# Kernel tuning notes

Hardware: AMD Instinct MI355X
Metric: run time of the kernel (lower is better)

Reference implementation:

```python
import jax, jax.numpy as jnp
import numpy as np

N_AST, M, C, D, H, OUT = 200000, 400000, 25000, 256, 4, 256


def setup_inputs() -> dict:
    key = jax.random.key(0)
    ks = jax.random.split(key, 12)
    s = 0.02
    return {
        "ast_nodes_encodings": jax.random.normal(ks[0], (N_AST, D), jnp.float32),
        "ast_node_idx_to_pdg_node_idx_mapping_key": jax.random.randint(ks[1], (M,), 0, N_AST),
        "ast_node_idx_to_pdg_node_idx_mapping_value": jax.random.randint(ks[2], (M,), 0, C),
        "pdg_node_idx_to_sub_ast_root_idx_mapping_key": jax.random.randint(ks[3], (C,), 0, C),
        "pdg_node_idx_to_sub_ast_root_idx_mapping_value": jax.random.randint(ks[4], (C,), 0, N_AST),
        "nr_cfg_nodes": C,
        "Wq": jax.random.normal(ks[5], (D, D), jnp.float32) * s,
        "bq": jnp.zeros((D,), jnp.float32),
        "Wk": jax.random.normal(ks[6], (D, D), jnp.float32) * s,
        "bk": jnp.zeros((D,), jnp.float32),
        "Wv": jax.random.normal(ks[7], (D, D), jnp.float32) * s,
        "bv": jnp.zeros((D,), jnp.float32),
        "Wo": jax.random.normal(ks[8], (D, OUT), jnp.float32) * s,
        "bo": jnp.zeros((OUT,), jnp.float32),
    }


def _scatter_attn(x, attn_keys, seg, num_segments, Wq, bq, Wk, bk, Wv, bv, Wo, bo):
    # x: [M, D] scattered inputs; attn_keys: [C, D] per-segment queries; seg: [M] segment ids.
    d_h = D // H
    q = (attn_keys @ Wq + bq).reshape(num_segments, H, d_h)  # [C,H,dh]
    k = (x @ Wk + bk).reshape(-1, H, d_h)                    # [M,H,dh]
    v = (x @ Wv + bv).reshape(-1, H, d_h)                    # [M,H,dh]
    scale = 1.0 / jnp.sqrt(jnp.asarray(d_h, x.dtype))
    scores = jnp.einsum('mhd,mhd->mh', k, q[seg]) * scale    # [M,H]
    m = jax.ops.segment_max(scores, seg, num_segments=num_segments)  # [C,H]
    e = jnp.exp(scores - m[seg])                             # [M,H]
    denom = jax.ops.segment_sum(e, seg, num_segments=num_segments)  # [C,H]
    num = jax.ops.segment_sum((e[..., None] * v).reshape(-1, H * d_h),
                              seg, num_segments=num_segments)        # [C,D]
    pooled = (num.reshape(num_segments, H, d_h) / (denom[..., None] + 1e-9)).reshape(num_segments, D)
    return pooled @ Wo + bo                                  # [C,OUT]


def reference(ast_nodes_encodings,
              ast_node_idx_to_pdg_node_idx_mapping_key,
              ast_node_idx_to_pdg_node_idx_mapping_value,
              pdg_node_idx_to_sub_ast_root_idx_mapping_key,
              pdg_node_idx_to_sub_ast_root_idx_mapping_value,
              nr_cfg_nodes, Wq, bq, Wk, bk, Wv, bv, Wo, bo):
    # Build per-CFG-node attention keys: gather sub-AST-root encodings, scatter by PDG node idx.
    root_enc = ast_nodes_encodings[pdg_node_idx_to_sub_ast_root_idx_mapping_value]  # [C,D]
    attn_keys = jnp.zeros((nr_cfg_nodes, D), ast_nodes_encodings.dtype)
    attn_keys = attn_keys.at[pdg_node_idx_to_sub_ast_root_idx_mapping_key].set(root_enc)
    # Gather AST node encodings per mapping entry and attention-pool per CFG node.
    scattered = ast_nodes_encodings[ast_node_idx_to_pdg_node_idx_mapping_key]       # [M,D]
    return _scatter_attn(scattered, attn_keys, ast_node_idx_to_pdg_node_idx_mapping_value,
                         nr_cfg_nodes, Wq, bq, Wk, bk, Wv, bv, Wo, bo)
```

## Files before the change

### kernel.cpp

```cpp
#include <hip/hip_runtime.h>
#include <hip/hip_bf16.h>
#include <math.h>

#define D 256
#define H 4
#define DH 64
#define NOUT 256

typedef short bf16x8 __attribute__((ext_vector_type(8)));
typedef float f32x4 __attribute__((ext_vector_type(4)));

__device__ __forceinline__ ushort f2bf(float f){
  uint b = __float_as_uint(f);
  b += 0x7FFF + ((b >> 16) & 1);
  return (ushort)(b >> 16);
}
__device__ __forceinline__ float bf2f(ushort u){
  return __uint_as_float(((uint)u) << 16);
}

__device__ __forceinline__ float redux32(float v){
  int t;
  t = __builtin_amdgcn_update_dpp(0, __float_as_int(v), 0x121, 0xF, 0xF, true); v += __int_as_float(t);
  t = __builtin_amdgcn_update_dpp(0, __float_as_int(v), 0x122, 0xF, 0xF, true); v += __int_as_float(t);
  t = __builtin_amdgcn_update_dpp(0, __float_as_int(v), 0x124, 0xF, 0xF, true); v += __int_as_float(t);
  t = __builtin_amdgcn_update_dpp(0, __float_as_int(v), 0x128, 0xF, 0xF, true); v += __int_as_float(t);
  v += __shfl_xor(v, 16, 64);
  return v;
}

__global__ void count_winner_kernel(const int* __restrict__ seg, int* __restrict__ counts,
                                    const int* __restrict__ pdgkey, int* __restrict__ winner,
                                    int M, int C){
  int i = blockIdx.x*256 + threadIdx.x;
  if (i < M){ int s = seg[i]; if (s >= 0 && s < C) atomicAdd(&counts[s], 1); }
  if (i < C){ int t = pdgkey[i]; if (t >= 0 && t < C) atomicMax(&winner[t], i); }
}

__global__ __launch_bounds__(1024) void scan1_kernel(const int* __restrict__ counts,
    int* __restrict__ loc, int* __restrict__ btot, int C){
  __shared__ int wtot[16];
  __shared__ int wexcl[16];
  int tid = threadIdx.x, lane = tid & 63, wv = tid >> 6;
  int i = blockIdx.x*1024 + tid;
  int v = (i < C) ? counts[i] : 0;
  int x = v;
  #pragma unroll
  for (int d2 = 1; d2 < 64; d2 <<= 1){
    int t = __shfl_up(x, d2, 64);
    if (lane >= d2) x += t;
  }
  if (lane == 63) wtot[wv] = x;
  __syncthreads();
  if (wv == 0 && lane < 16){
    int t = wtot[lane]; int y = t;
    #pragma unroll
    for (int d2 = 1; d2 < 16; d2 <<= 1){
      int u = __shfl_up(y, d2, 64);
      if (lane >= d2) y += u;
    }
    wexcl[lane] = y - t;
    if (lane == 15) btot[blockIdx.x] = y;
  }
  __syncthreads();
  if (i < C) loc[i] = wexcl[wv] + x - v;
}

__global__ void scan2_kernel(const int* __restrict__ btot, int* __restrict__ bexcl,
                             int nb, int* __restrict__ offsets, int C){
  int lane = threadIdx.x;
  int v = (lane < nb) ? btot[lane] : 0;
  int x = v;
  #pragma unroll
  for (int d2 = 1; d2 < 64; d2 <<= 1){
    int t = __shfl_up(x, d2, 64);
    if (lane >= d2) x += t;
  }
  if (lane < nb) bexcl[lane] = x - v;
  if (lane == 63) offsets[C] = x;
}

__global__ void scan3_kernel(const int* __restrict__ loc, const int* __restrict__ bexcl,
                             int* __restrict__ offsets, int* __restrict__ pos, int C){
  int i = blockIdx.x*256 + threadIdx.x;
  if (i < C){ int o = loc[i] + bexcl[i >> 10]; offsets[i] = o; pos[i] = o; }
}

__global__ void fill_kernel(const int* __restrict__ seg, const int* __restrict__ astkey,
                            int* __restrict__ pos, int* __restrict__ rows, int M, int C){
  int i = blockIdx.x*256 + threadIdx.x;
  if (i < M){
    int s = seg[i];
    if (s >= 0 && s < C){ int p = atomicAdd(&pos[s], 1); rows[p] = astkey[i]; }
  }
}

__global__ __launch_bounds__(256) void prep_weights(
    const float* __restrict__ Wq, const float* __restrict__ Wk,
    const float* __restrict__ Wv, const float* __restrict__ Wo,
    const float* __restrict__ bq, const float* __restrict__ bk,
    const float* __restrict__ bv,
    ushort* __restrict__ Wq16, ushort* __restrict__ Wk16, ushort* __restrict__ Wv16,
    ushort* __restrict__ WoT16,
    float* __restrict__ wqbk, float* __restrict__ bvo,
    float* __restrict__ bqk, float* __restrict__ cbh){
  __shared__ float t[64][65];
  int bid = blockIdx.x, tid = threadIdx.x;
  if (bid < 256){
    int id = bid*256 + tid;
    Wq16[id] = f2bf(Wq[id]);
    Wk16[id] = f2bf(Wk[id]);
    Wv16[id] = f2bf(Wv[id]);
  } else if (bid < 269){
    int id = (bid - 256)*256 + tid;
    if (id < 1024){
      int h = id >> 8, k = id & 255;
      float s = 0.f;
      for (int d = 0; d < DH; d++) s += Wq[(size_t)k*256 + h*64 + d] * bk[h*64 + d];
      wqbk[id] = s;
    } else if (id < 2048){
      int tt = id - 1024; int h = tt >> 8, o = tt & 255;
      float s = 0.f;
      for (int d = 0; d < DH; d++) s += bv[h*64 + d] * Wo[(size_t)(h*64 + d)*256 + o];
      bvo[tt] = s;
    } else if (id < 3072){
      int tt = id - 2048; int h = tt >> 8, e = tt & 255;
      float s = 0.f;
      for (int d = 0; d < DH; d++) s += bq[h*64 + d] * Wk[(size_t)e*256 + h*64 + d];
      bqk[tt] = s;
    } else if (id < 3076){
      int h = id - 3072;
      float s = 0.f;
      for (int d = 0; d < DH; d++) s += bq[h*64 + d] * bk[h*64 + d];
      cbh[h] = s;
    }
  } else {
    int b2 = bid - 269;
    int bx = b2 & 3, by = b2 >> 2;
    int r = tid >> 6, cc = tid & 63;
    #pragma unroll
    for (int rr = 0; rr < 64; rr += 4)
      t[rr + r][cc] = Wo[(size_t)(by*64 + rr + r)*256 + bx*64 + cc];
    __syncthreads();
    #pragma unroll
    for (int rr = 0; rr < 64; rr += 4)
      WoT16[(size_t)(bx*64 + rr + r)*256 + by*64 + cc] = f2bf(t[cc][rr + r]);
  }
}

__global__ void gather_ag(const float* __restrict__ enc, const int* __restrict__ rootval,
                          const int* __restrict__ winner,
                          const float* __restrict__ wqbk, const float* __restrict__ cbh,
                          ushort* __restrict__ Ag, float* __restrict__ qb, int C){
  int id = blockIdx.x*256 + threadIdx.x;
  int c = id >> 6, g = id & 63;
  if (c >= C) return;
  int w = winner[c];
  float4 v = make_float4(0.f, 0.f, 0.f, 0.f);
  if (w >= 0) v = *(const float4*)(enc + (size_t)rootval[w]*D + g*4);
  ushort4 u; u.x = f2bf(v.x); u.y = f2bf(v.y); u.z = f2bf(v.z); u.w = f2bf(v.w);
  *(ushort4*)(Ag + (size_t)c*D + g*4) = u;
  float b0 = bf2f(u.x), b1 = bf2f(u.y), b2 = bf2f(u.z), b3 = bf2f(u.w);
  float pv[4];
  #pragma unroll
  for (int h = 0; h < 4; h++){
    float4 wv = *(const float4*)(wqbk + h*256 + g*4);
    float p = b0*wv.x + b1*wv.y + b2*wv.z + b3*wv.w;
    p = redux32(p);
    p += __shfl_xor(p, 32, 64);
    pv[h] = p;
  }
  if (g < 4) qb[c*4 + g] = pv[g] + cbh[g];
}

template<bool OUT_BF16>
__global__ __launch_bounds__(256) void mfma_gemm(
    const ushort* __restrict__ A, int sA, int acol_h,
    const ushort* __restrict__ Bt, int sBt, int btrow_h, int btcol_h,
    void* __restrict__ Out, int sOut, int outrow_h, int outcol_h,
    int M, int K,
    const float* __restrict__ bias, const float* __restrict__ beta4,
    const float* __restrict__ bvo4){
  __shared__ __align__(16) ushort As[64][72];
  __shared__ __align__(16) ushort Bs[64][72];
  int tid = threadIdx.x;
  int hz = blockIdx.z;
  int m0 = blockIdx.x*64;
  int acol0  = acol_h*hz;
  int btrow0 = blockIdx.y*64 + btrow_h*hz;
  int btcol0 = btcol_h*hz;
  int outrow0 = outrow_h*hz;
  int outcol0 = blockIdx.y*64 + outcol_h*hz;
  int w = tid >> 6, lane = tid & 63, quad = lane >> 4, l16 = lane & 15;
  int r1 = tid >> 3, c8 = (tid & 7)*8;
  f32x4 acc[4] = {};
  for (int k0 = 0; k0 < K; k0 += 64){
    const ushort* ga = A + (size_t)(m0 + r1)*sA + acol0 + k0 + c8;
    uint4 v1 = make_uint4(0,0,0,0), v2 = make_uint4(0,0,0,0);
    if (m0 + r1 < M)      v1 = *(const uint4*)ga;
    if (m0 + r1 + 32 < M) v2 = *(const uint4*)(ga + (size_t)32*sA);
    *(uint4*)&As[r1][c8]      = v1;
    *(uint4*)&As[r1+32][c8]   = v2;
    const ushort* gb = Bt + (size_t)(btrow0 + r1)*sBt + btcol0 + k0 + c8;
    *(uint4*)&Bs[r1][c8]      = *(const uint4*)gb;
    *(uint4*)&Bs[r1+32][c8]   = *(const uint4*)(gb + (size_t)32*sBt);
    __syncthreads();
    #pragma unroll
    for (int ks = 0; ks < 2; ks++){
      bf16x8 b = *(const bf16x8*)&Bs[w*16 + l16][ks*32 + quad*8];
      #pragma unroll
      for (int mt = 0; mt < 4; mt++){
        bf16x8 a = *(const bf16x8*)&As[mt*16 + l16][ks*32 + quad*8];
        acc[mt] = __builtin_amdgcn_mfma_f32_16x16x32_bf16(a, b, acc[mt], 0, 0, 0);
      }
    }
    __syncthreads();
  }
  int col = outcol0 + w*16 + l16;
  int bcol = btrow0 + w*16 + l16;
  float bval = bias ? bias[bcol] : 0.f;
  #pragma unroll
  for (int mt = 0; mt < 4; mt++){
    #pragma unroll
    for (int r = 0; r < 4; r++){
      int row = m0 + mt*16 + quad*4 + r;
      if (row < M){
        float v = acc[mt][r] + bval;
        if (bvo4){
          v += beta4[row*4+0]*bvo4[0*256 + bcol] + beta4[row*4+1]*bvo4[1*256 + bcol]
             + beta4[row*4+2]*bvo4[2*256 + bcol] + beta4[row*4+3]*bvo4[3*256 + bcol];
        }
        if (OUT_BF16) ((ushort*)Out)[(size_t)(outrow0 + row)*sOut + col] = f2bf(v);
        else          ((float*)Out)[(size_t)(outrow0 + row)*sOut + col] = v;
      }
    }
  }
}

__global__ __launch_bounds__(256) void seg_attn(const float* __restrict__ enc,
    const int* __restrict__ rows, const int* __restrict__ offsets,
    const ushort* __restrict__ qk16, const float* __restrict__ qb,
    ushort* __restrict__ Shat16, float* __restrict__ beta, int C){
  int lane = threadIdx.x & 63, wave = threadIdx.x >> 6;
  int half = lane >> 5, sl = lane & 31;
  int c = blockIdx.x*8 + wave*2 + half;
  if (c >= C) return;
  float qk[4][8];
  const ushort* qkp = qk16 + (size_t)c*1024 + sl*8;
  #pragma unroll
  for (int h = 0; h < 4; h++){
    uint4 u = *(const uint4*)(qkp + h*256);
    qk[h][0]=__uint_as_float(u.x<<16); qk[h][1]=__uint_as_float(u.x&0xffff0000u);
    qk[h][2]=__uint_as_float(u.y<<16); qk[h][3]=__uint_as_float(u.y&0xffff0000u);
    qk[h][4]=__uint_as_float(u.z<<16); qk[h][5]=__uint_as_float(u.z&0xffff0000u);
    qk[h][6]=__uint_as_float(u.w<<16); qk[h][7]=__uint_as_float(u.w&0xffff0000u);
  }
  float4 qbv = *(const float4*)(qb + (size_t)c*4);
  float qbh[4] = {qbv.x, qbv.y, qbv.z, qbv.w};
  int off = offsets[c];
  int n = offsets[c+1] - off;
  float S[4][8] = {};
  float l[4] = {0.f, 0.f, 0.f, 0.f};
  for (int base = 0; base < n; base += 32){
    int cnt = min(32, n - base);
    int xrow = 0;
    if (sl < cnt) xrow = rows[off + base + sl];
    int r0 = __shfl(xrow, half*32 + 0, 64);
    int r1 = __shfl(xrow, half*32 + ((cnt > 1) ? 1 : 0), 64);
    const float* p0 = enc + (size_t)r0*256 + sl*8;
    const float* p1 = enc + (size_t)r1*256 + sl*8;
    float4 xa0 = *(const float4*)p0, xa1 = *(const float4*)(p0 + 4);
    float4 xb0 = *(const float4*)p1, xb1 = *(const float4*)(p1 + 4);
    for (int j = 0; j < cnt; j += 2){
      float4 na0 = xa0, na1 = xa1, nb0 = xb0, nb1 = xb1;
      if (j + 2 < cnt){
        int rr0 = __shfl(xrow, half*32 + j + 2, 64);
        int rr1 = __shfl(xrow, half*32 + ((j + 3 < cnt) ? (j + 3) : (j + 2)), 64);
        const float* q0 = enc + (size_t)rr0*256 + sl*8;
        const float* q1 = enc + (size_t)rr1*256 + sl*8;
        na0 = *(const float4*)q0; na1 = *(const float4*)(q0 + 4);
        nb0 = *(const float4*)q1; nb1 = *(const float4*)(q1 + 4);
      }
      float xa[8] = {xa0.x, xa0.y, xa0.z, xa0.w, xa1.x, xa1.y, xa1.z, xa1.w};
      float xb[8] = {xb0.x, xb0.y, xb0.z, xb0.w, xb1.x, xb1.y, xb1.z, xb1.w};
      float pa[4], pb[4];
      #pragma unroll
      for (int h = 0; h < 4; h++){
        pa[h] = xa[0]*qk[h][0] + xa[1]*qk[h][1] + xa[2]*qk[h][2] + xa[3]*qk[h][3]
              + xa[4]*qk[h][4] + xa[5]*qk[h][5] + xa[6]*qk[h][6] + xa[7]*qk[h][7];
        pb[h] = xb[0]*qk[h][0] + xb[1]*qk[h][1] + xb[2]*qk[h][2] + xb[3]*qk[h][3]
              + xb[4]*qk[h][4] + xb[5]*qk[h][5] + xb[6]*qk[h][6] + xb[7]*qk[h][7];
      }
      #pragma unroll
      for (int h = 0; h < 4; h++){ pa[h] = redux32(pa[h]); pb[h] = redux32(pb[h]); }
      bool v1 = (j + 1) < cnt;
      float ea[4], eb[4];
      #pragma unroll
      for (int h = 0; h < 4; h++){
        ea[h] = __expf((pa[h] + qbh[h]) * 0.125f);
        eb[h] = v1 ? __expf((pb[h] + qbh[h]) * 0.125f) : 0.f;
      }
      #pragma unroll
      for (int h = 0; h < 4; h++){
        l[h] += ea[h] + eb[h];
        #pragma unroll
        for (int k = 0; k < 8; k++){
          S[h][k] += ea[h]*xa[k];
          S[h][k] += eb[h]*xb[k];
        }
      }
      xa0 = na0; xa1 = na1; xb0 = nb0; xb1 = nb1;
    }
  }
  float inv[4];
  #pragma unroll
  for (int h = 0; h < 4; h++) inv[h] = 1.f / (l[h] + 1e-9f);
  ushort* sp = Shat16 + (size_t)c*1024 + sl*8;
  #pragma unroll
  for (int h = 0; h < 4; h++){
    float ih = inv[h];
    uint4 o;
    o.x = (uint)f2bf(S[h][0]*ih) | ((uint)f2bf(S[h][1]*ih) << 16);
    o.y = (uint)f2bf(S[h][2]*ih) | ((uint)f2bf(S[h][3]*ih) << 16);
    o.z = (uint)f2bf(S[h][4]*ih) | ((uint)f2bf(S[h][5]*ih) << 16);
    o.w = (uint)f2bf(S[h][6]*ih) | ((uint)f2bf(S[h][7]*ih) << 16);
    *(uint4*)(sp + h*256) = o;
  }
  if (sl == 0){
    beta[c*4+0] = l[0] / (l[0] + 1e-9f);
    beta[c*4+1] = l[1] / (l[1] + 1e-9f);
    beta[c*4+2] = l[2] / (l[2] + 1e-9f);
    beta[c*4+3] = l[3] / (l[3] + 1e-9f);
  }
}

extern "C" void kernel_launch(void* const* d_in, const int* in_sizes, int n_in,
                              void* d_out, int out_size, void* d_ws, size_t ws_size,
                              hipStream_t stream) {
  const float* enc    = (const float*)d_in[0];
  const int*   astkey = (const int*)d_in[1];
  const int*   seg    = (const int*)d_in[2];
  const int*   pdgkey = (const int*)d_in[3];
  const int*   pdgval = (const int*)d_in[4];
  const float* Wq = (const float*)d_in[6];
  const float* bq = (const float*)d_in[7];
  const float* Wk = (const float*)d_in[8];
  const float* bk = (const float*)d_in[9];
  const float* Wv = (const float*)d_in[10];
  const float* bv = (const float*)d_in[11];
  const float* Wo = (const float*)d_in[12];
  const float* bo = (const float*)d_in[13];
  float* out = (float*)d_out;
  const int M = in_sizes[1];
  const int C = in_sizes[3];

  char* p = (char*)d_ws;
  auto alloc = [&](size_t bytes) -> void* {
    void* r = (void*)p;
    p += (bytes + 255) / 256 * 256;
    return r;
  };
  ushort* Ag      = (ushort*)alloc((size_t)C * D * 2);
  ushort* qk16    = (ushort*)alloc((size_t)C * H * D * 2);
  ushort* Shat16  = (ushort*)alloc((size_t)C * H * D * 2);
  float*  beta    = (float*)alloc((size_t)C * H * 4);
  float*  qb      = (float*)alloc((size_t)C * H * 4);
  ushort* Wq16    = (ushort*)alloc((size_t)D * D * 2);
  ushort* Wk16    = (ushort*)alloc((size_t)D * D * 2);
  ushort* Wv16    = (ushort*)alloc((size_t)D * D * 2);
  ushort* WoT16   = (ushort*)alloc((size_t)D * D * 2);
  ushort* Gt16    = (ushort*)alloc((size_t)H * D * D * 2);
  ushort* Zt16    = (ushort*)alloc((size_t)D * H * D * 2);
  float*  wqbk    = (float*)alloc((size_t)H * D * 4);
  float*  bvo     = (float*)alloc((size_t)H * NOUT * 4);
  float*  bqk     = (float*)alloc((size_t)H * D * 4);
  float*  cbh     = (float*)alloc((size_t)H * 4);
  int*   winner   = (int*)alloc((size_t)C * 4);
  int*   counts   = (int*)alloc((size_t)C * 4);
  int*   loc      = (int*)alloc((size_t)C * 4);
  int*   btot     = (int*)alloc((size_t)64 * 4);
  int*   bexcl    = (int*)alloc((size_t)64 * 4);
  int*   offsets  = (int*)alloc((size_t)(C + 1) * 4);
  int*   pos      = (int*)alloc((size_t)C * 4);
  int*   rows     = (int*)alloc((size_t)M * 4);

  hipMemsetAsync(winner, 0xFF, (size_t)C * 4, stream);
  hipMemsetAsync(counts, 0, (size_t)C * 4, stream);

  int gC = (C + 255) / 256, gM = (M + 255) / 256;
  int gMC = ((M > C ? M : C) + 255) / 256;
  int nb1024 = (C + 1023) / 1024;
  count_winner_kernel<<<gMC, 256, 0, stream>>>(seg, counts, pdgkey, winner, M, C);
  scan1_kernel<<<nb1024, 1024, 0, stream>>>(counts, loc, btot, C);
  scan2_kernel<<<1, 64, 0, stream>>>(btot, bexcl, nb1024, offsets, C);
  scan3_kernel<<<gC, 256, 0, stream>>>(loc, bexcl, offsets, pos, C);
  fill_kernel<<<gM, 256, 0, stream>>>(seg, astkey, pos, rows, M, C);

  prep_weights<<<285, 256, 0, stream>>>(Wq, Wk, Wv, Wo, bq, bk, bv,
                                        Wq16, Wk16, Wv16, WoT16, wqbk, bvo, bqk, cbh);

  mfma_gemm<true><<<dim3(4,4,4), 256, 0, stream>>>(
      Wk16, D, DH,  Wq16, D, 0, DH,  Gt16, D, D, 0,  D, DH, nullptr, nullptr, nullptr);
  mfma_gemm<true><<<dim3(4,4,4), 256, 0, stream>>>(
      WoT16, D, DH,  Wv16, D, 0, DH,  Zt16, H*D, 0, D,  D, DH, nullptr, nullptr, nullptr);

  gather_ag<<<(C*64 + 255)/256, 256, 0, stream>>>(enc, pdgval, winner, wqbk, cbh,
                                                  Ag, qb, C);

  int mt = (C + 63) / 64;
  mfma_gemm<true><<<dim3(mt,4,4), 256, 0, stream>>>(
      Ag, D, 0,  Gt16, D, D, 0,  qk16, H*D, 0, D,  C, D, bqk, nullptr, nullptr);

  seg_attn<<<(C + 7)/8, 256, 0, stream>>>(enc, rows, offsets, qk16, qb,
                                          Shat16, beta, C);

  mfma_gemm<false><<<dim3(mt,4,1), 256, 0, stream>>>(
      Shat16, H*D, 0,  Zt16, H*D, 0, 0,  out, NOUT, 0, 0,  C, H*D, bo, beta, bvo);
}
```

Before: 500.4 us.

## Replace 64-row MFMA GEMMs with 128x128 tiled GEMM kernel

Adds a gemm128 kernel in which each block computes a 128x128 output tile. Its four waves each hold a 4x4 grid of 16x16 MFMA accumulators and stage 64-wide K slices of A and B in shared memory. This kernel replaces the older 64-row mfma_gemm for the C x 1024 qk projection and the C x 256 output projection. The aim is more operand reuse per shared-memory load and fewer global reads. The A buffers are padded to a multiple of 128 rows so the loads need no bounds checks, but those padded rows are never initialised and may hold garbage; the row guard on stores keeps them out of the output.

```diff
diff --git a/kernel.cpp b/kernel.cpp
--- a/kernel.cpp
+++ b/kernel.cpp
@@ -237,6 +237,77 @@
   }
 }
 
+template<bool OUT_BF16>
+__global__ __launch_bounds__(256) void gemm128(
+    const ushort* __restrict__ A, int sA,
+    const ushort* __restrict__ Bt, int sBt,
+    void* __restrict__ Out, int sOut,
+    int Mrows, int K,
+    const float* __restrict__ bias, const float* __restrict__ beta4,
+    const float* __restrict__ bvo4){
+  __shared__ __align__(16) ushort As[128][72];
+  __shared__ __align__(16) ushort Bs[128][72];
+  int tid = threadIdx.x;
+  int m0 = blockIdx.x*128, n0 = blockIdx.y*128;
+  int wave = tid >> 6, lane = tid & 63, quad = lane >> 4, l16 = lane & 15;
+  int wr = (wave >> 1)*64, wc = (wave & 1)*64;
+  int r1 = tid >> 3, c8 = (tid & 7)*8;
+  f32x4 acc[4][4] = {};
+  const ushort* ga0 = A + (size_t)(m0 + r1)*sA + c8;
+  const ushort* gb0 = Bt + (size_t)(n0 + r1)*sBt + c8;
+  for (int k0 = 0; k0 < K; k0 += 64){
+    const ushort* ga = ga0 + k0;
+    const ushort* gb = gb0 + k0;
+    #pragma unroll
+    for (int rr = 0; rr < 128; rr += 32){
+      *(uint4*)&As[r1 + rr][c8] = *(const uint4*)(ga + (size_t)rr*sA);
+      *(uint4*)&Bs[r1 + rr][c8] = *(const uint4*)(gb + (size_t)rr*sBt);
+    }
+    __syncthreads();
+    #pragma unroll
+    for (int ks = 0; ks < 2; ks++){
+      bf16x8 b[4], a[4];
+      #pragma unroll
+      for (int nt = 0; nt < 4; nt++) b[nt] = *(const bf16x8*)&Bs[wc + nt*16 + l16][ks*32 + quad*8];
+      #pragma unroll
+      for (int mt = 0; mt < 4; mt++) a[mt] = *(const bf16x8*)&As[wr + mt*16 + l16][ks*32 + quad*8];
+      #pragma unroll
+      for (int mt = 0; mt < 4; mt++){
+        #pragma unroll
+        for (int nt = 0; nt < 4; nt++)
+          acc[mt][nt] = __builtin_amdgcn_mfma_f32_16x16x32_bf16(a[mt], b[nt], acc[mt][nt], 0, 0, 0);
+      }
+    }
+    __syncthreads();
+  }
+  #pragma unroll
+  for (int nt = 0; nt < 4; nt++){
+    int col = n0 + wc + nt*16 + l16;
+    float bval = bias ? bias[col] : 0.f;
+    float bv0 = 0.f, bv1 = 0.f, bv2 = 0.f, bv3 = 0.f;
+    if (bvo4){
+      bv0 = bvo4[0*256 + col]; bv1 = bvo4[1*256 + col];
+      bv2 = bvo4[2*256 + col]; bv3 = bvo4[3*256 + col];
+    }
+    #pragma unroll
+    for (int mt = 0; mt < 4; mt++){
+      #pragma unroll
+      for (int r = 0; r < 4; r++){
+        int row = m0 + wr + mt*16 + quad*4 + r;
+        if (row < Mrows){
+          float v = acc[mt][nt][r] + bval;
+          if (bvo4){
+            v += beta4[row*4+0]*bv0 + beta4[row*4+1]*bv1
+               + beta4[row*4+2]*bv2 + beta4[row*4+3]*bv3;
+          }
+          if (OUT_BF16) ((ushort*)Out)[(size_t)row*sOut + col] = f2bf(v);
+          else          ((float*)Out)[(size_t)row*sOut + col] = v;
+        }
+      }
+    }
+  }
+}
+
 __global__ __launch_bounds__(256) void seg_attn(const float* __restrict__ enc,
     const int* __restrict__ rows, const int* __restrict__ offsets,
     const ushort* __restrict__ qk16, const float* __restrict__ qb,
@@ -353,6 +424,8 @@
   float* out = (float*)d_out;
   const int M = in_sizes[1];
   const int C = in_sizes[3];
+  const int mt128 = (C + 127) / 128;
+  const int Cpad = mt128 * 128;
 
   char* p = (char*)d_ws;
   auto alloc = [&](size_t bytes) -> void* {
@@ -360,9 +433,9 @@
     p += (bytes + 255) / 256 * 256;
     return r;
   };
-  ushort* Ag      = (ushort*)alloc((size_t)C * D * 2);
+  ushort* Ag      = (ushort*)alloc((size_t)Cpad * D * 2);
   ushort* qk16    = (ushort*)alloc((size_t)C * H * D * 2);
-  ushort* Shat16  = (ushort*)alloc((size_t)C * H * D * 2);
+  ushort* Shat16  = (ushort*)alloc((size_t)Cpad * H * D * 2);
   float*  beta    = (float*)alloc((size_t)C * H * 4);
   float*  qb      = (float*)alloc((size_t)C * H * 4);
   ushort* Wq16    = (ushort*)alloc((size_t)D * D * 2);
@@ -407,13 +480,12 @@
   gather_ag<<<(C*64 + 255)/256, 256, 0, stream>>>(enc, pdgval, winner, wqbk, cbh,
                                                   Ag, qb, C);
 
-  int mt = (C + 63) / 64;
-  mfma_gemm<true><<<dim3(mt,4,4), 256, 0, stream>>>(
-      Ag, D, 0,  Gt16, D, D, 0,  qk16, H*D, 0, D,  C, D, bqk, nullptr, nullptr);
+  gemm128<true><<<dim3(mt128, (H*D)/128), 256, 0, stream>>>(
+      Ag, D,  Gt16, D,  qk16, H*D,  C, D,  bqk, nullptr, nullptr);
 
   seg_attn<<<(C + 7)/8, 256, 0, stream>>>(enc, rows, offsets, qk16, qb,
                                           Shat16, beta, C);
 
-  mfma_gemm<false><<<dim3(mt,4,1), 256, 0, stream>>>(
-      Shat16, H*D, 0,  Zt16, H*D, 0, 0,  out, NOUT, 0, 0,  C, H*D, bo, beta, bvo);
-}
+  gemm128<false><<<dim3(mt128, NOUT/128), 256, 0, stream>>>(
+      Shat16, H*D,  Zt16, H*D,  out, NOUT,  C, H*D,  bo, beta, bvo);
+}
```

Measured after the change: 518.0 us. +3.5%, slower.
